# Kernel optimization log

Measured on AMD Instinct MI355X. Metric: run time of the kernel, lower is better.

The kernel has to match this reference:

```python
import jax, jax.numpy as jnp
import numpy as np

I_DIM = 20000        # item (node) count; emb_mat has I_DIM+1 rows
EMB_DIM = 128        # input embedding dim
D_DIM = 128          # hidden (scaled) dim
N_EDGES = 640000     # number of (src, dst) edges


def setup_inputs() -> dict:
    key = jax.random.key(0)
    k1, k2, k3, k4 = jax.random.split(key, 4)
    emb_mat = jax.random.normal(k1, (I_DIM + 1, EMB_DIM), dtype=jnp.float32)
    # edges must be sorted by source node (column 0) so that the original
    # tf.repeat(segment_sums, bincount(src)) trick is well-defined.
    edge = jax.random.randint(k2, (N_EDGES, 2), 0, I_DIM + 1, dtype=jnp.int64)
    order = jnp.argsort(edge[:, 0])
    edge = edge[order]
    W_scale = jax.random.normal(k3, (EMB_DIM, D_DIM), dtype=jnp.float32) * 0.05
    b_scale = jnp.zeros((D_DIM,), dtype=jnp.float32)
    W_att = jax.random.normal(k4, (2 * D_DIM, 1), dtype=jnp.float32) * 0.05
    b_att = jnp.zeros((1,), dtype=jnp.float32)
    return {"emb_mat": emb_mat, "edge": edge, "W_scale": W_scale,
            "b_scale": b_scale, "W_att": W_att, "b_att": b_att}


def reference(emb_mat, edge, W_scale, b_scale, W_att, b_att):
    num_segments = emb_mat.shape[0]          # i_dim + 1
    seg = edge[:, 0]                         # source nodes (segment ids), [E]

    # gather both endpoints, scale: [E, 2, emb] -> [E, 2, d]
    edge_emb = emb_mat[edge] @ W_scale + b_scale
    E = edge_emb.shape[0]
    # attention logit per edge from concatenated endpoint features
    att = (edge_emb.reshape(E, -1) @ W_att + b_att)[:, 0]   # [E]
    att = jax.nn.leaky_relu(att, negative_slope=0.2)
    scores = jnp.exp(att - 1.0)                              # exp(att - ones)

    # manual segment softmax over edges grouped by source node
    score_sum = jax.ops.segment_sum(scores, seg, num_segments=num_segments)
    score_norm = scores / score_sum[seg]                     # [E]

    # scale all node embeddings once, gather destination features
    item_scaled = emb_mat @ W_scale + b_scale                # [N, d]
    items = item_scaled[edge[:, 1]]                          # [E, d]

    agg = jax.ops.segment_sum(score_norm[:, None] * items, seg,
                              num_segments=num_segments)     # [N, d]
    return jax.nn.sigmoid(agg)
```

## Files before the change

### kernel.cpp

```cpp
#include <hip/hip_runtime.h>
#include <math.h>

#define NSEG 20001
#define EMB  128
#define NE   640000

#define SCALE_BLOCKS ((NSEG + 15) / 16)
#define BOUNDS_BLOCKS ((NE + 255) / 256)

__device__ __forceinline__ float dot4(float4 a, float4 b) {
    return a.x*b.x + a.y*b.y + a.z*b.z + a.w*b.w;
}

#define FMA4(acc, s, b) { acc.x += (s)*(b).x; acc.y += (s)*(b).y; acc.z += (s)*(b).z; acc.w += (s)*(b).w; }

__device__ __forceinline__ unsigned short f2bf(float x) {
    unsigned u = __float_as_uint(x);
    unsigned r = (u + 0x7fffu + ((u >> 16) & 1u)) >> 16;
    return (unsigned short)r;
}

__global__ __launch_bounds__(256) void prep_kernel(
    const float* __restrict__ emb, const float* __restrict__ W,
    const float* __restrict__ bsc, const float* __restrict__ Watt,
    const int* __restrict__ edge,
    unsigned short* __restrict__ tab,
    float* __restrict__ a_src, float* __restrict__ a_dst,
    int* __restrict__ seg_start)
{
    const int tid = threadIdx.x;
    if (blockIdx.x >= SCALE_BLOCKS) {
        int e = (blockIdx.x - SCALE_BLOCKS) * 256 + tid;
        if (e >= NE) return;
        int s  = edge[2*e];
        int sp = (e == 0) ? -1 : edge[2*e - 2];
        for (int t = sp + 1; t <= s; ++t) seg_start[t] = e;
        if (e == NE - 1) {
            for (int t = s + 1; t <= NSEG; ++t) seg_start[t] = NE;
        }
        return;
    }

    __shared__ float emb_s[16 * EMB];
    const int r0 = blockIdx.x * 16;

    const float4* embg4 = (const float4*)emb;
    float4* es4 = (float4*)emb_s;
    const int gmax = NSEG * 32 - 1;
    #pragma unroll
    for (int j = 0; j < 2; ++j) {
        int idx = tid + j * 256;
        int g = r0 * 32 + idx;
        es4[idx] = embg4[g <= gmax ? g : gmax];
    }
    __syncthreads();

    const int cg = tid & 31;
    const int rb = (tid >> 5) * 2;

    float4 acc0 = {0.f,0.f,0.f,0.f};
    float4 acc1 = {0.f,0.f,0.f,0.f};
    const float4* Wg4 = (const float4*)W;

    for (int k = 0; k < EMB; k += 4) {
        float4 b0 = Wg4[(k+0)*32 + cg];
        float4 b1 = Wg4[(k+1)*32 + cg];
        float4 b2 = Wg4[(k+2)*32 + cg];
        float4 b3 = Wg4[(k+3)*32 + cg];
        float4 a0 = *(const float4*)&emb_s[(rb+0)*EMB + k];
        float4 a1 = *(const float4*)&emb_s[(rb+1)*EMB + k];
        FMA4(acc0, a0.x, b0); FMA4(acc0, a0.y, b1); FMA4(acc0, a0.z, b2); FMA4(acc0, a0.w, b3);
        FMA4(acc1, a1.x, b0); FMA4(acc1, a1.y, b1); FMA4(acc1, a1.z, b2); FMA4(acc1, a1.w, b3);
    }

    float4 bs = *(const float4*)&bsc[cg*4];
    acc0.x += bs.x; acc0.y += bs.y; acc0.z += bs.z; acc0.w += bs.w;
    acc1.x += bs.x; acc1.y += bs.y; acc1.z += bs.z; acc1.w += bs.w;

    const int row0 = r0 + rb;
    const int row1 = row0 + 1;
    if (row0 < NSEG) {
        ushort4 p = { f2bf(acc0.x), f2bf(acc0.y), f2bf(acc0.z), f2bf(acc0.w) };
        *(ushort4*)&tab[row0*EMB + cg*4] = p;
    }
    if (row1 < NSEG) {
        ushort4 p = { f2bf(acc1.x), f2bf(acc1.y), f2bf(acc1.z), f2bf(acc1.w) };
        *(ushort4*)&tab[row1*EMB + cg*4] = p;
    }

    float4 ws = *(const float4*)&Watt[cg*4];
    float4 wd = *(const float4*)&Watt[EMB + cg*4];
    float p0s = dot4(acc0, ws), p0d = dot4(acc0, wd);
    float p1s = dot4(acc1, ws), p1d = dot4(acc1, wd);
    #pragma unroll
    for (int off = 16; off >= 1; off >>= 1) {
        p0s += __shfl_xor(p0s, off);
        p0d += __shfl_xor(p0d, off);
        p1s += __shfl_xor(p1s, off);
        p1d += __shfl_xor(p1d, off);
    }
    if ((tid & 31) == 0) {
        if (row0 < NSEG) { a_src[row0] = p0s; a_dst[row0] = p0d; }
        if (row1 < NSEG) { a_src[row1] = p1s; a_dst[row1] = p1d; }
    }
}

__device__ __forceinline__ float bcastf(float v, int j) {
    return __uint_as_float(__builtin_amdgcn_readlane(__float_as_uint(v), j));
}
__device__ __forceinline__ float bf_lo(unsigned u) { return __uint_as_float(u << 16); }
__device__ __forceinline__ float bf_hi(unsigned u) { return __uint_as_float(u & 0xffff0000u); }

__global__ __launch_bounds__(256) void agg_kernel(
    const int* __restrict__ edge, const float* __restrict__ a_src,
    const float* __restrict__ a_dst, const float* __restrict__ b_att,
    const int* __restrict__ seg_start, const unsigned int* __restrict__ tab32,
    float* __restrict__ out)
{
    const int wid = blockIdx.x * 4 + (threadIdx.x >> 6);
    if (wid >= NSEG) return;
    const int lane = threadIdx.x & 63;
    const unsigned int* tabl = tab32 + lane;

    const int s0 = seg_start[wid];
    const int s1 = seg_start[wid + 1];
    const float aS = a_src[wid] + b_att[0];

    float accx = 0.f, accy = 0.f, ssum = 0.f;

    for (int cb = s0; cb < s1; cb += 64) {
        int n = s1 - cb; if (n > 64) n = 64;
        int e = cb + lane;
        int dmine = 0; float sc = 0.f;
        if (lane < n) {
            dmine = edge[2*e + 1] << 6;
            float att = aS + a_dst[dmine >> 6];
            att = att > 0.f ? att : 0.2f * att;
            sc  = expf(att - 1.f);
        }
        ssum += sc;

        int j = 0;
        for (; j + 3 < n; j += 4) {
            float w0 = bcastf(sc, j+0), w1 = bcastf(sc, j+1);
            float w2 = bcastf(sc, j+2), w3 = bcastf(sc, j+3);
            int d0 = __builtin_amdgcn_readlane(dmine, j+0);
            int d1 = __builtin_amdgcn_readlane(dmine, j+1);
            int d2 = __builtin_amdgcn_readlane(dmine, j+2);
            int d3 = __builtin_amdgcn_readlane(dmine, j+3);
            unsigned u0 = tabl[d0];
            unsigned u1 = tabl[d1];
            unsigned u2 = tabl[d2];
            unsigned u3 = tabl[d3];
            accx += w0 * bf_lo(u0); accy += w0 * bf_hi(u0);
            accx += w1 * bf_lo(u1); accy += w1 * bf_hi(u1);
            accx += w2 * bf_lo(u2); accy += w2 * bf_hi(u2);
            accx += w3 * bf_lo(u3); accy += w3 * bf_hi(u3);
        }
        for (; j < n; ++j) {
            float w = bcastf(sc, j);
            int   d = __builtin_amdgcn_readlane(dmine, j);
            unsigned u = tabl[d];
            accx += w * bf_lo(u);
            accy += w * bf_hi(u);
        }
    }

    #pragma unroll
    for (int off = 32; off >= 1; off >>= 1) ssum += __shfl_xor(ssum, off);

    const float inv = (s1 > s0) ? 1.f / ssum : 0.f;
    float ox = accx * inv, oy = accy * inv;
    ox = 1.f / (1.f + expf(-ox));
    oy = 1.f / (1.f + expf(-oy));
    *(float2*)&out[wid * EMB + 2 * lane] = make_float2(ox, oy);
}

extern "C" void kernel_launch(void* const* d_in, const int* in_sizes, int n_in,
                              void* d_out, int out_size, void* d_ws, size_t ws_size,
                              hipStream_t stream) {
    const float* emb  = (const float*)d_in[0];
    const int*   edge = (const int*)  d_in[1];
    const float* W    = (const float*)d_in[2];
    const float* bsc  = (const float*)d_in[3];
    const float* Watt = (const float*)d_in[4];
    const float* batt = (const float*)d_in[5];
    float* out = (float*)d_out;

    unsigned short* tab = (unsigned short*)d_ws;
    float* a_src = (float*)(tab + (size_t)NSEG * EMB);
    float* a_dst = a_src + NSEG;
    int*   seg_start = (int*)(a_dst + NSEG);

    prep_kernel<<<SCALE_BLOCKS + BOUNDS_BLOCKS, 256, 0, stream>>>(
        emb, W, bsc, Watt, edge, tab, a_src, a_dst, seg_start);
    agg_kernel<<<(NSEG + 3) / 4, 256, 0, stream>>>(
        edge, a_src, a_dst, batt, seg_start, (const unsigned int*)tab, out);
}
```

Baseline: 116.1 us.

## Gather four edges per wave with 16-byte row loads and compact dst indices

The aggregation kernel now splits each 64-lane wave into four 16-lane groups. Each group handles a different edge, and each lane loads 16 bytes (eight bf16 values) of the destination row. Partial sums are then reduced across the groups with xor shuffles. This replaces one narrow 4-byte load per lane per edge with wide vector loads and cuts loop iterations about fourfold. The prep kernel also writes a compact dst index array, using shfl_up to get the previous source id, so aggregation no longer reads the interleaved edge pairs. The costs are extra cross-lane reductions, only 16 lanes doing the output stores, and wasted work on padded tail edges when a segment's edge count is not a multiple of four.

```diff
diff --git a/kernel.cpp b/kernel.cpp
--- a/kernel.cpp
+++ b/kernel.cpp
@@ -6,7 +6,7 @@
 #define NE   640000
 
 #define SCALE_BLOCKS ((NSEG + 15) / 16)
-#define BOUNDS_BLOCKS ((NE + 255) / 256)
+#define BOUNDS_BLOCKS (NE / 256)
 
 __device__ __forceinline__ float dot4(float4 a, float4 b) {
     return a.x*b.x + a.y*b.y + a.z*b.z + a.w*b.w;
@@ -26,17 +26,18 @@
     const int* __restrict__ edge,
     unsigned short* __restrict__ tab,
     float* __restrict__ a_src, float* __restrict__ a_dst,
-    int* __restrict__ seg_start)
+    int* __restrict__ seg_start, int* __restrict__ dst)
 {
     const int tid = threadIdx.x;
     if (blockIdx.x >= SCALE_BLOCKS) {
         int e = (blockIdx.x - SCALE_BLOCKS) * 256 + tid;
-        if (e >= NE) return;
-        int s  = edge[2*e];
-        int sp = (e == 0) ? -1 : edge[2*e - 2];
-        for (int t = sp + 1; t <= s; ++t) seg_start[t] = e;
+        int2 p = ((const int2*)edge)[e];
+        dst[e] = p.y;
+        int sp = __shfl_up(p.x, 1);
+        if ((tid & 63) == 0) sp = (e == 0) ? -1 : edge[2*e - 2];
+        for (int t = sp + 1; t <= p.x; ++t) seg_start[t] = e;
         if (e == NE - 1) {
-            for (int t = s + 1; t <= NSEG; ++t) seg_start[t] = NE;
+            for (int t = p.x + 1; t <= NSEG; ++t) seg_start[t] = NE;
         }
         return;
     }
@@ -105,75 +106,74 @@
     }
 }
 
-__device__ __forceinline__ float bcastf(float v, int j) {
-    return __uint_as_float(__builtin_amdgcn_readlane(__float_as_uint(v), j));
-}
 __device__ __forceinline__ float bf_lo(unsigned u) { return __uint_as_float(u << 16); }
 __device__ __forceinline__ float bf_hi(unsigned u) { return __uint_as_float(u & 0xffff0000u); }
 
 __global__ __launch_bounds__(256) void agg_kernel(
-    const int* __restrict__ edge, const float* __restrict__ a_src,
+    const int* __restrict__ dst, const float* __restrict__ a_src,
     const float* __restrict__ a_dst, const float* __restrict__ b_att,
-    const int* __restrict__ seg_start, const unsigned int* __restrict__ tab32,
+    const int* __restrict__ seg_start, const unsigned char* __restrict__ tabb,
     float* __restrict__ out)
 {
     const int wid = blockIdx.x * 4 + (threadIdx.x >> 6);
     if (wid >= NSEG) return;
     const int lane = threadIdx.x & 63;
-    const unsigned int* tabl = tab32 + lane;
+    const int quad = lane >> 4;
+    const int qoff = (lane & 15) * 16;
 
     const int s0 = seg_start[wid];
     const int s1 = seg_start[wid + 1];
     const float aS = a_src[wid] + b_att[0];
 
-    float accx = 0.f, accy = 0.f, ssum = 0.f;
+    float c0=0.f,c1=0.f,c2=0.f,c3=0.f,c4=0.f,c5=0.f,c6=0.f,c7=0.f;
+    float ssum = 0.f;
 
     for (int cb = s0; cb < s1; cb += 64) {
         int n = s1 - cb; if (n > 64) n = 64;
         int e = cb + lane;
         int dmine = 0; float sc = 0.f;
         if (lane < n) {
-            dmine = edge[2*e + 1] << 6;
-            float att = aS + a_dst[dmine >> 6];
+            dmine = dst[e];
+            float att = aS + a_dst[dmine];
             att = att > 0.f ? att : 0.2f * att;
             sc  = expf(att - 1.f);
         }
         ssum += sc;
 
-        int j = 0;
-        for (; j + 3 < n; j += 4) {
-            float w0 = bcastf(sc, j+0), w1 = bcastf(sc, j+1);
-            float w2 = bcastf(sc, j+2), w3 = bcastf(sc, j+3);
-            int d0 = __builtin_amdgcn_readlane(dmine, j+0);
-            int d1 = __builtin_amdgcn_readlane(dmine, j+1);
-            int d2 = __builtin_amdgcn_readlane(dmine, j+2);
-            int d3 = __builtin_amdgcn_readlane(dmine, j+3);
-            unsigned u0 = tabl[d0];
-            unsigned u1 = tabl[d1];
-            unsigned u2 = tabl[d2];
-            unsigned u3 = tabl[d3];
-            accx += w0 * bf_lo(u0); accy += w0 * bf_hi(u0);
-            accx += w1 * bf_lo(u1); accy += w1 * bf_hi(u1);
-            accx += w2 * bf_lo(u2); accy += w2 * bf_hi(u2);
-            accx += w3 * bf_lo(u3); accy += w3 * bf_hi(u3);
+        #pragma unroll 4
+        for (int j = 0; j < n; j += 4) {
+            float w = __shfl(sc, j + quad, 64);
+            int   d = __shfl(dmine, j + quad, 64);
+            uint4 u = *(const uint4*)(tabb + ((size_t)(unsigned)((d << 8) + qoff)));
+            c0 += w * bf_lo(u.x); c1 += w * bf_hi(u.x);
+            c2 += w * bf_lo(u.y); c3 += w * bf_hi(u.y);
+            c4 += w * bf_lo(u.z); c5 += w * bf_hi(u.z);
+            c6 += w * bf_lo(u.w); c7 += w * bf_hi(u.w);
         }
-        for (; j < n; ++j) {
-            float w = bcastf(sc, j);
-            int   d = __builtin_amdgcn_readlane(dmine, j);
-            unsigned u = tabl[d];
-            accx += w * bf_lo(u);
-            accy += w * bf_hi(u);
-        }
     }
 
     #pragma unroll
     for (int off = 32; off >= 1; off >>= 1) ssum += __shfl_xor(ssum, off);
 
+    #pragma unroll
+    for (int off = 16; off <= 32; off <<= 1) {
+        c0 += __shfl_xor(c0, off); c1 += __shfl_xor(c1, off);
+        c2 += __shfl_xor(c2, off); c3 += __shfl_xor(c3, off);
+        c4 += __shfl_xor(c4, off); c5 += __shfl_xor(c5, off);
+        c6 += __shfl_xor(c6, off); c7 += __shfl_xor(c7, off);
+    }
+
     const float inv = (s1 > s0) ? 1.f / ssum : 0.f;
-    float ox = accx * inv, oy = accy * inv;
-    ox = 1.f / (1.f + expf(-ox));
-    oy = 1.f / (1.f + expf(-oy));
-    *(float2*)&out[wid * EMB + 2 * lane] = make_float2(ox, oy);
+    if (lane < 16) {
+        float4 o0, o1;
+        o0.x = 1.f/(1.f+expf(-c0*inv)); o0.y = 1.f/(1.f+expf(-c1*inv));
+        o0.z = 1.f/(1.f+expf(-c2*inv)); o0.w = 1.f/(1.f+expf(-c3*inv));
+        o1.x = 1.f/(1.f+expf(-c4*inv)); o1.y = 1.f/(1.f+expf(-c5*inv));
+        o1.z = 1.f/(1.f+expf(-c6*inv)); o1.w = 1.f/(1.f+expf(-c7*inv));
+        float4* op = (float4*)&out[wid * EMB + lane * 8];
+        op[0] = o0;
+        op[1] = o1;
+    }
 }
 
 extern "C" void kernel_launch(void* const* d_in, const int* in_sizes, int n_in,
@@ -191,9 +191,10 @@
     float* a_src = (float*)(tab + (size_t)NSEG * EMB);
     float* a_dst = a_src + NSEG;
     int*   seg_start = (int*)(a_dst + NSEG);
+    int*   dstc = seg_start + NSEG + 3;
 
     prep_kernel<<<SCALE_BLOCKS + BOUNDS_BLOCKS, 256, 0, stream>>>(
-        emb, W, bsc, Watt, edge, tab, a_src, a_dst, seg_start);
+        emb, W, bsc, Watt, edge, tab, a_src, a_dst, seg_start, dstc);
     agg_kernel<<<(NSEG + 3) / 4, 256, 0, stream>>>(
-        edge, a_src, a_dst, batt, seg_start, (const unsigned int*)tab, out);
-}
+        dstc, a_src, a_dst, batt, seg_start, (const unsigned char*)tab, out);
+}
```

New measurement: 118.5 us. +2.0%, slower.
